# Optimization experiments

Hardware: AMD Instinct MI355X
Metric: run time of the kernel (lower is better)

The kernel has to match this reference:

```python
import jax, jax.numpy as jnp
import numpy as np

PH, PW, PS = 4, 4, 16          # patch grid h/w and patch_size
SEQ = PS * PS                  # 256 tokens per chunk
EH = EW = ET = 4               # mem_expand_size
RPW = 2 * EW + 1               # 9
RPH = 2 * EH + 1               # 9
RPF = RPH * RPW                # 81
HEADS, DHEAD, DIM = 16, 64, 1024
INNER = HEADS * DHEAD
SCALE = DHEAD ** -0.5


def _pos(idx):
    nf = PH * PW
    inner = idx % nf
    return inner % PH, inner // PH, idx // nf


def _rotary(freqs, t):
    # freqs: [n, rot_dim] broadcast over leading dims of t [..., n, rot_dim]
    x1 = t[..., 0::2]
    x2 = t[..., 1::2]
    rot = jnp.stack((-x2, x1), axis=-1).reshape(t.shape)
    return t * jnp.cos(freqs) + rot * jnp.sin(freqs)


def setup_inputs() -> dict:
    key = jax.random.key(0)
    ks = jax.random.split(key, 9)
    B, M, TXT = 16, 8, 77
    KV = M * SEQ + TXT
    return {
        "x": jax.random.normal(ks[0], (B, SEQ, DIM), jnp.float32),
        "cond": jax.random.normal(ks[1], (B, KV, DIM), jnp.float32),
        "freqs": jax.random.normal(ks[2], (PH * PS, PW * PS, DHEAD), jnp.float32),
        "Wq": jax.random.normal(ks[3], (DIM, INNER), jnp.float32) * 0.02,
        "Wk": jax.random.normal(ks[4], (DIM, INNER), jnp.float32) * 0.02,
        "Wv": jax.random.normal(ks[5], (DIM, INNER), jnp.float32) * 0.02,
        "rel_table": jax.random.normal(ks[6], (RPH * RPW * (2 * ET + 1), HEADS), jnp.float32) * 0.02,
        "Wo": jax.random.normal(ks[7], (INNER, DIM), jnp.float32) * 0.02,
        "bo": jax.random.normal(ks[8], (DIM,), jnp.float32) * 0.02,
        "mem_idxs": jnp.arange(8, dtype=jnp.int64) if jax.config.jax_enable_x64 else jnp.arange(8, dtype=jnp.int32),
        "cur_patch_idx": 21,
    }


def reference(x, cond, freqs, Wq, Wk, Wv, rel_table, Wo, bo, mem_idxs, cur_patch_idx):
    B = x.shape[0]
    M = mem_idxs.shape[0]
    MS = M * SEQ
    # QKV projections -> [b, h, n, d]
    q = (x @ Wq).reshape(B, SEQ, HEADS, DHEAD).transpose(0, 2, 1, 3)
    k = (cond @ Wk).reshape(B, -1, HEADS, DHEAD).transpose(0, 2, 1, 3)
    v = (cond @ Wv).reshape(B, -1, HEADS, DHEAD).transpose(0, 2, 1, 3)

    # relative position indices (gather into bias table)
    rs, cs, ts = _pos(cur_patch_idx)           # python ints (static)
    rt, ct, tt = _pos(mem_idxs)                # [M] arrays
    rel_idx = (rt - rs + EH) * RPW + (ct - cs + EW) + (tt - ts + ET) * RPF
    bias = rel_table[rel_idx]                  # [M, H]
    bias = jnp.repeat(bias.T, SEQ, axis=1)[None, :, :, None]  # [1, H, M*SEQ, 1]
    km = k[:, :, :MS] + bias                   # bias added to memory K before rotary

    # rotary freqs: source patch (static slice) and target patches (gathered)
    src = freqs[rs * PS:(rs + 1) * PS, cs * PS:(cs + 1) * PS].reshape(SEQ, -1)
    rows = rt[:, None] * PS + jnp.arange(PS)   # [M, PS]
    cols = ct[:, None] * PS + jnp.arange(PS)   # [M, PS]
    tgt = freqs[rows[:, :, None], cols[:, None, :]].reshape(MS, -1)  # [M*SEQ, rot]

    q = _rotary(src, q)
    km = _rotary(tgt, km)
    k = jnp.concatenate([km, k[:, :, MS:]], axis=2)

    dots = jnp.einsum('bhid,bhjd->bhij', q, k) * SCALE
    attn = jax.nn.softmax(dots, axis=-1)
    out = jnp.einsum('bhij,bhjd->bhid', attn, v)
    out = out.transpose(0, 2, 1, 3).reshape(B, SEQ, INNER)
    return out @ Wo + bo
```

## Files before the change

### kernel.cpp

```cpp
#include <hip/hip_runtime.h>
#include <cstdint>

typedef __bf16 bf16;
typedef bf16 bf16x2 __attribute__((ext_vector_type(2)));
typedef bf16 bf16x4 __attribute__((ext_vector_type(4)));
typedef bf16 bf16x8 __attribute__((ext_vector_type(8)));
typedef float floatx4 __attribute__((ext_vector_type(4)));

#define SEQ   256
#define DIMM  1024
#define HEADS 16
#define KV_LEN 2125
#define KV_PAD 2176
#define KV_BLKS 17
#define MS_TOK 2048
#define ATT_SCALE 0.125f
#define TILE_ELEMS (128 * 32)

__device__ __forceinline__ void load_lds16(const bf16* g, bf16* l) {
    __builtin_amdgcn_global_load_lds(
        (const __attribute__((address_space(1))) void*)g,
        (__attribute__((address_space(3))) void*)l, 16, 0, 0);
}

__global__ __launch_bounds__(256) void convert_kernel(
        const float* __restrict__ src, bf16* __restrict__ dst, long total) {
    long i4 = ((long)blockIdx.x * 256 + threadIdx.x) * 4;
    if (i4 >= total) return;
    const float4 v = *(const float4*)(src + i4);
    bf16x4 o;
    o[0] = (bf16)v.x; o[1] = (bf16)v.y; o[2] = (bf16)v.z; o[3] = (bf16)v.w;
    *(bf16x4*)(dst + i4) = o;
}

__global__ __launch_bounds__(256) void convert_cond_kernel(
        const float* __restrict__ src, bf16* __restrict__ dst, long total_dst) {
    long i4 = ((long)blockIdx.x * 256 + threadIdx.x) * 4;
    if (i4 >= total_dst) return;
    long drow = i4 >> 10;
    int b = (int)(drow / KV_PAD);
    int j = (int)(drow - (long)b * KV_PAD);
    bf16x4 o;
    if (j < KV_LEN) {
        long srow = (long)b * KV_LEN + j;
        const float4 v = *(const float4*)(src + (srow << 10) + (i4 & 1023));
        o[0] = (bf16)v.x; o[1] = (bf16)v.y; o[2] = (bf16)v.z; o[3] = (bf16)v.w;
    } else {
        o[0] = o[1] = o[2] = o[3] = (bf16)0.f;
    }
    *(bf16x4*)(dst + i4) = o;
}

__global__ __launch_bounds__(256) void transpose_bf16_kernel(
        const float* __restrict__ W, bf16* __restrict__ Wt, int N) {
    __shared__ float tile[32][33];
    int n0 = blockIdx.x * 32, k0 = blockIdx.y * 32;
    int r = threadIdx.x >> 5, c = threadIdx.x & 31;
    #pragma unroll
    for (int i = 0; i < 4; ++i)
        tile[r + i * 8][c] = W[(size_t)(k0 + r + i * 8) * N + n0 + c];
    __syncthreads();
    #pragma unroll
    for (int i = 0; i < 4; ++i)
        Wt[(size_t)(n0 + r + i * 8) * N + k0 + c] = (bf16)tile[c][r + i * 8];
}

__global__ __launch_bounds__(256) void rot_tables_kernel(
        const float* __restrict__ freqs, const float* __restrict__ rel_table,
        const int* __restrict__ mem_idxs, const int* __restrict__ cur,
        float* __restrict__ ckT, float* __restrict__ skT,
        float* __restrict__ cqT, float* __restrict__ sqT,
        float* __restrict__ biasK) {
    int t = blockIdx.x * 256 + threadIdx.x;
    const int cp = *cur; const int inner = cp & 15;
    const int rs = inner & 3, cs = inner >> 2, ts = cp >> 4;
    if (t < MS_TOK * 64) {
        int j = t >> 6, d = t & 63;
        int mi = mem_idxs[j >> 8];
        int rt = mi & 3, ct = (mi >> 2) & 3;
        int pidx = j & 255;
        int fr = rt * 16 + (pidx >> 4), fc = ct * 16 + (pidx & 15);
        float f = freqs[(size_t)(fr * 64 + fc) * 64 + d];
        ckT[t] = __cosf(f); skT[t] = __sinf(f);
    } else if (t < MS_TOK * 64 + SEQ * 64) {
        int t2 = t - MS_TOK * 64;
        int s = t2 >> 6, d = t2 & 63;
        int fr = rs * 16 + (s >> 4), fc = cs * 16 + (s & 15);
        float f = freqs[(size_t)(fr * 64 + fc) * 64 + d];
        cqT[t2] = __cosf(f); sqT[t2] = __sinf(f);
    } else if (t < MS_TOK * 64 + SEQ * 64 + 128) {
        int t3 = t - (MS_TOK * 64 + SEQ * 64);
        int m = t3 >> 4, h = t3 & 15;
        int mi = mem_idxs[m];
        int rt = mi & 3, ct = (mi >> 2) & 3, tt = mi >> 4;
        int rel = (rt - rs + 4) * 9 + (ct - cs + 4) + (tt - ts + 4) * 81;
        biasK[t3] = rel_table[rel * HEADS + h];
    }
}

__device__ __forceinline__ void gemm_loop_db(
        const bf16* __restrict__ Ag, const bf16* __restrict__ Bg, int K,
        bf16* __restrict__ As, bf16* __restrict__ Bs,
        floatx4 (&acc)[4][4]) {
    const int tid  = threadIdx.x;
    const int wave = tid >> 6, lane = tid & 63;
    const int quad = lane >> 4, l16 = lane & 15;
    const int wm = wave >> 1, wn = wave & 1;
    #pragma unroll
    for (int i = 0; i < 2; ++i) {
        int c = i * 256 + wave * 64 + lane;
        int r = c >> 2, c8 = (c & 3) * 8;
        load_lds16(Ag + (long)r * K + c8, As + (i * 256 + wave * 64) * 8);
        load_lds16(Bg + (long)r * K + c8, Bs + (i * 256 + wave * 64) * 8);
    }
    for (int k0 = 0; k0 < K; k0 += 32) {
        const int cur = (k0 >> 5) & 1;
        bf16* Asc = As + cur * TILE_ELEMS;
        bf16* Bsc = Bs + cur * TILE_ELEMS;
        __syncthreads();
        if (k0 + 32 < K) {
            bf16* Asn = As + (cur ^ 1) * TILE_ELEMS;
            bf16* Bsn = Bs + (cur ^ 1) * TILE_ELEMS;
            #pragma unroll
            for (int i = 0; i < 2; ++i) {
                int c = i * 256 + wave * 64 + lane;
                int r = c >> 2, c8 = (c & 3) * 8;
                load_lds16(Ag + (long)r * K + k0 + 32 + c8, Asn + (i * 256 + wave * 64) * 8);
                load_lds16(Bg + (long)r * K + k0 + 32 + c8, Bsn + (i * 256 + wave * 64) * 8);
            }
        }
        bf16x8 af[4], bfr[4];
        #pragma unroll
        for (int mt = 0; mt < 4; ++mt)
            af[mt] = *(const bf16x8*)(Asc + (wm * 64 + mt * 16 + l16) * 32 + quad * 8);
        #pragma unroll
        for (int nt = 0; nt < 4; ++nt)
            bfr[nt] = *(const bf16x8*)(Bsc + (wn * 64 + nt * 16 + l16) * 32 + quad * 8);
        #pragma unroll
        for (int mt = 0; mt < 4; ++mt)
            #pragma unroll
            for (int nt = 0; nt < 4; ++nt)
                acc[mt][nt] = __builtin_amdgcn_mfma_f32_16x16x32_bf16(af[mt], bfr[nt], acc[mt][nt], 0, 0, 0);
    }
}

__global__ __launch_bounds__(256) void gemm_o_kernel(
        const bf16* __restrict__ A, const bf16* __restrict__ Bt,
        float* __restrict__ Cout, const float* __restrict__ bias, int N) {
    __shared__ bf16 As[2 * TILE_ELEMS];
    __shared__ bf16 Bs[2 * TILE_ELEMS];
    const int tid  = threadIdx.x;
    const int wave = tid >> 6, lane = tid & 63;
    const int quad = lane >> 4, l16 = lane & 15;
    const int wm = wave >> 1, wn = wave & 1;
    const long row0 = (long)blockIdx.x * 128, col0 = (long)blockIdx.y * 128;
    floatx4 acc[4][4] = {};
    gemm_loop_db(A + row0 * DIMM, Bt + col0 * DIMM, DIMM, As, Bs, acc);
    #pragma unroll
    for (int mt = 0; mt < 4; ++mt) {
        #pragma unroll
        for (int nt = 0; nt < 4; ++nt) {
            long r = row0 + wm * 64 + mt * 16 + quad * 4;
            long ccol = col0 + wn * 64 + nt * 16 + l16;
            float bv = bias[ccol];
            #pragma unroll
            for (int i = 0; i < 4; ++i)
                Cout[(r + i) * (long)N + ccol] = acc[mt][nt][i] + bv;
        }
    }
}

__global__ __launch_bounds__(256) void gemm_q_rot_kernel(
        const bf16* __restrict__ A, const bf16* __restrict__ Bt,
        bf16* __restrict__ Qout, const float* __restrict__ cqT,
        const float* __restrict__ sqT) {
    __shared__ bf16 As[2 * TILE_ELEMS];
    __shared__ bf16 Bs[2 * TILE_ELEMS];
    const int tid  = threadIdx.x;
    const int wave = tid >> 6, lane = tid & 63;
    const int quad = lane >> 4, l16 = lane & 15;
    const int wm = wave >> 1, wn = wave & 1;
    const long row0 = (long)blockIdx.x * 128, col0 = (long)blockIdx.y * 128;
    floatx4 acc[4][4] = {};
    gemm_loop_db(A + row0 * DIMM, Bt + col0 * DIMM, DIMM, As, Bs, acc);
    #pragma unroll
    for (int mt = 0; mt < 4; ++mt) {
        #pragma unroll
        for (int nt = 0; nt < 4; ++nt) {
            long rr = row0 + wm * 64 + mt * 16 + quad * 4;
            int ccol = (int)col0 + wn * 64 + nt * 16 + l16;
            int d = ccol & 63;
            #pragma unroll
            for (int i = 0; i < 4; ++i) {
                long r = rr + i; int s = (int)(r & 255);
                float c_ = cqT[s * 64 + d], s_ = sqT[s * 64 + d];
                float q = acc[mt][nt][i];
                float pn = __shfl_xor(q, 1);
                float outv = (d & 1) ? (q * c_ + pn * s_) : (q * c_ - pn * s_);
                Qout[r * DIMM + ccol] = (bf16)outv;
            }
        }
    }
}

__global__ __launch_bounds__(256) void gemm_k_kernel(
        const bf16* __restrict__ A, const bf16* __restrict__ Btk,
        bf16* __restrict__ Kout, const float* __restrict__ ckT,
        const float* __restrict__ skT, const float* __restrict__ biasK) {
    __shared__ bf16 As[2 * TILE_ELEMS];
    __shared__ bf16 Bs[2 * TILE_ELEMS];
    const int tid  = threadIdx.x;
    const int wave = tid >> 6, lane = tid & 63;
    const int quad = lane >> 4, l16 = lane & 15;
    const int wm = wave >> 1, wn = wave & 1;
    const long row0 = (long)blockIdx.x * 128, col0 = (long)blockIdx.y * 128;
    floatx4 acc[4][4] = {};
    gemm_loop_db(A + row0 * DIMM, Btk + col0 * DIMM, DIMM, As, Bs, acc);
    const int bidx = (int)(row0 / KV_PAD);
    #pragma unroll
    for (int mt = 0; mt < 4; ++mt) {
        #pragma unroll
        for (int nt = 0; nt < 4; ++nt) {
            long rr = row0 + wm * 64 + mt * 16 + quad * 4;
            int ccol = (int)col0 + wn * 64 + nt * 16 + l16;
            int h = ccol >> 6, d = ccol & 63;
            int jbase = (int)(rr - (long)bidx * KV_PAD);
            #pragma unroll
            for (int i = 0; i < 4; ++i) {
                int j = jbase + i;
                float kb = acc[mt][nt][i];
                float c_ = 1.f, s_ = 0.f;
                if (j < MS_TOK) {
                    kb += biasK[((j >> 8) << 4) + h];
                    c_ = ckT[j * 64 + d]; s_ = skT[j * 64 + d];
                }
                float pn = __shfl_xor(kb, 1);
                float outv = (d & 1) ? (kb * c_ + pn * s_) : (kb * c_ - pn * s_);
                Kout[(rr + i) * DIMM + ccol] = (bf16)outv;
            }
        }
    }
}

__global__ __launch_bounds__(256) void gemm_vt_kernel(
        const bf16* __restrict__ Wvt, const bf16* __restrict__ condb,
        bf16* __restrict__ VT) {
    __shared__ bf16 As[2 * TILE_ELEMS];
    __shared__ bf16 Bs[2 * TILE_ELEMS];
    const int tid  = threadIdx.x;
    const int wave = tid >> 6, lane = tid & 63;
    const int quad = lane >> 4, l16 = lane & 15;
    const int wm = wave >> 1, wn = wave & 1;
    const int b  = blockIdx.y / KV_BLKS, tb = blockIdx.y % KV_BLKS;
    const long row0 = (long)blockIdx.x * 128;
    const long col0 = (long)tb * 128;
    const bf16* Bt = condb + (size_t)b * KV_PAD * DIMM;
    floatx4 acc[4][4] = {};
    gemm_loop_db(Wvt + row0 * DIMM, Bt + col0 * DIMM, DIMM, As, Bs, acc);
    #pragma unroll
    for (int mt = 0; mt < 4; ++mt) {
        #pragma unroll
        for (int nt = 0; nt < 4; ++nt) {
            long f0 = row0 + wm * 64 + mt * 16 + quad * 4;
            long t0 = col0 + wn * 64 + nt * 16 + l16;
            #pragma unroll
            for (int i = 0; i < 4; ++i)
                VT[((size_t)b * DIMM + f0 + i) * KV_PAD + t0] = (bf16)acc[mt][nt][i];
        }
    }
}

__global__ __launch_bounds__(256, 3) void attn_kernel(
        const bf16* __restrict__ Qb, const bf16* __restrict__ Kb,
        const bf16* __restrict__ VT, bf16* __restrict__ Ob) {
    const int bh = blockIdx.x & 255, qt = blockIdx.x >> 8;
    const int b = bh >> 4, h = bh & 15;
    const int tid = threadIdx.x, wave = tid >> 6, lane = tid & 63;
    const int quad = lane >> 4, l16 = lane & 15;
    __shared__ bf16 Ks[128 * 72];
    __shared__ bf16 Vt[64 * 144];
    __shared__ bf16 Ps[4][16 * 72];

    const int qrow0 = b * SEQ + qt * 64 + wave * 16;
    const bf16* qp = Qb + (size_t)(qrow0 + l16) * DIMM + h * 64 + quad * 8;
    bf16x8 qf0 = *(const bf16x8*)(qp);
    bf16x8 qf1 = *(const bf16x8*)(qp + 32);

    floatx4 oacc[4] = {};
    floatx4 lacc = {};
    bf16x8 ones;
    #pragma unroll
    for (int t = 0; t < 8; ++t) ones[t] = (bf16)1.0f;

    const size_t kbase = ((size_t)b * KV_PAD) * DIMM + h * 64;
    const size_t vbase = ((size_t)(bh * 64)) * KV_PAD;

    const int kchunk = tid & 1;
    const int gl = tid >> 1;
    const int g  = ((gl & 31) << 2) | (gl >> 5);
    const int gg = g & 63;
    const int dstrow = (g >> 6) * 64 + ((gg & 3) << 4) + (gg >> 2);
    const int vd = tid >> 2, vseg = tid & 3;

    bf16x8 kr[4], vr[4];
    {
        int jr = g; if (jr > KV_LEN - 1) jr = KV_LEN - 1;
        const bf16* gp = Kb + kbase + (size_t)jr * DIMM + kchunk * 32;
        kr[0] = *(const bf16x8*)(gp);      kr[1] = *(const bf16x8*)(gp + 8);
        kr[2] = *(const bf16x8*)(gp + 16); kr[3] = *(const bf16x8*)(gp + 24);
        const bf16* vp = VT + vbase + (size_t)vd * KV_PAD + vseg * 32;
        vr[0] = *(const bf16x8*)(vp);      vr[1] = *(const bf16x8*)(vp + 8);
        vr[2] = *(const bf16x8*)(vp + 16); vr[3] = *(const bf16x8*)(vp + 24);
    }

    for (int j0 = 0; j0 < KV_LEN; j0 += 128) {
        __syncthreads();
        {
            bf16* dp = Ks + dstrow * 72 + kchunk * 32;
            *(bf16x8*)(dp)      = kr[0]; *(bf16x8*)(dp + 8)  = kr[1];
            *(bf16x8*)(dp + 16) = kr[2]; *(bf16x8*)(dp + 24) = kr[3];
            bf16* dv = Vt + vd * 144 + vseg * 32;
            *(bf16x8*)(dv)      = vr[0]; *(bf16x8*)(dv + 8)  = vr[1];
            *(bf16x8*)(dv + 16) = vr[2]; *(bf16x8*)(dv + 24) = vr[3];
        }
        __syncthreads();
        if (j0 + 128 < KV_LEN) {
            int jr = j0 + 128 + g; if (jr > KV_LEN - 1) jr = KV_LEN - 1;
            const bf16* gp = Kb + kbase + (size_t)jr * DIMM + kchunk * 32;
            kr[0] = *(const bf16x8*)(gp);      kr[1] = *(const bf16x8*)(gp + 8);
            kr[2] = *(const bf16x8*)(gp + 16); kr[3] = *(const bf16x8*)(gp + 24);
            const bf16* vp = VT + vbase + (size_t)vd * KV_PAD + j0 + 128 + vseg * 32;
            vr[0] = *(const bf16x8*)(vp);      vr[1] = *(const bf16x8*)(vp + 8);
            vr[2] = *(const bf16x8*)(vp + 16); vr[3] = *(const bf16x8*)(vp + 24);
        }
        #pragma unroll
        for (int c = 0; c < 2; ++c) {
            floatx4 s[4] = {};
            #pragma unroll
            for (int jt = 0; jt < 4; ++jt) {
                const bf16* kp = Ks + (c * 64 + jt * 16 + l16) * 72 + quad * 8;
                bf16x8 kb0 = *(const bf16x8*)(kp);
                bf16x8 kb1 = *(const bf16x8*)(kp + 32);
                s[jt] = __builtin_amdgcn_mfma_f32_16x16x32_bf16(qf0, kb0, s[jt], 0, 0, 0);
                s[jt] = __builtin_amdgcn_mfma_f32_16x16x32_bf16(qf1, kb1, s[jt], 0, 0, 0);
            }
            const int colbase = j0 + c * 64 + 4 * l16;
            #pragma unroll
            for (int r = 0; r < 4; ++r) {
                bf16x4 pk;
                #pragma unroll
                for (int jt = 0; jt < 4; ++jt) {
                    bool ok = (colbase + jt) < KV_LEN;
                    float p = ok ? __expf(s[jt][r] * ATT_SCALE) : 0.f;
                    pk[jt] = (bf16)p;
                }
                *(bf16x4*)(&Ps[wave][(quad * 4 + r) * 72 + l16 * 4]) = pk;
            }
            #pragma unroll
            for (int kf = 0; kf < 2; ++kf) {
                bf16x8 pa = *(const bf16x8*)(&Ps[wave][l16 * 72 + kf * 32 + quad * 8]);
                lacc = __builtin_amdgcn_mfma_f32_16x16x32_bf16(pa, ones, lacc, 0, 0, 0);
                #pragma unroll
                for (int dt = 0; dt < 4; ++dt) {
                    bf16x8 vb = *(const bf16x8*)(Vt + (dt * 16 + l16) * 144 + c * 64 + kf * 32 + quad * 8);
                    oacc[dt] = __builtin_amdgcn_mfma_f32_16x16x32_bf16(pa, vb, oacc[dt], 0, 0, 0);
                }
            }
        }
    }
    #pragma unroll
    for (int r = 0; r < 4; ++r) {
        float inv = 1.f / lacc[r];
        size_t orow = (size_t)(qrow0 + quad * 4 + r) * DIMM + h * 64;
        #pragma unroll
        for (int dt = 0; dt < 4; ++dt)
            Ob[orow + dt * 16 + l16] = (bf16)(oacc[dt][r] * inv);
    }
}

extern "C" void kernel_launch(void* const* d_in, const int* in_sizes, int n_in,
                              void* d_out, int out_size, void* d_ws, size_t ws_size,
                              hipStream_t stream) {
    const float* x     = (const float*)d_in[0];
    const float* cond  = (const float*)d_in[1];
    const float* freqs = (const float*)d_in[2];
    const float* Wq    = (const float*)d_in[3];
    const float* Wk    = (const float*)d_in[4];
    const float* Wv    = (const float*)d_in[5];
    const float* rel   = (const float*)d_in[6];
    const float* Wo    = (const float*)d_in[7];
    const float* bo    = (const float*)d_in[8];
    const int* mem_idxs = (const int*)d_in[9];
    const int* cur      = (const int*)d_in[10];
    float* out = (float*)d_out;

    const int B   = 16;
    const int Mq  = B * SEQ;
    const int Mkv_pad = B * KV_PAD;

    char* ws = (char*)d_ws;
    size_t off = 0;
    auto alloc = [&](size_t bytes) { void* pp = ws + off; off = (off + bytes + 255) & ~(size_t)255; return pp; };
    bf16* xb    = (bf16*)alloc((size_t)Mq * DIMM * 2);
    bf16* condb = (bf16*)alloc((size_t)Mkv_pad * DIMM * 2);
    bf16* Wqt   = (bf16*)alloc((size_t)DIMM * DIMM * 2);
    bf16* Wkt   = (bf16*)alloc((size_t)DIMM * DIMM * 2);
    bf16* Wvt   = (bf16*)alloc((size_t)DIMM * DIMM * 2);
    bf16* Wot   = (bf16*)alloc((size_t)DIMM * DIMM * 2);
    bf16* Qb    = (bf16*)alloc((size_t)Mq * DIMM * 2);
    bf16* Kb    = (bf16*)alloc((size_t)Mkv_pad * DIMM * 2);
    bf16* VTb   = (bf16*)alloc((size_t)B * DIMM * KV_PAD * 2);
    bf16* Ab    = (bf16*)alloc((size_t)Mq * DIMM * 2);
    float* ckT  = (float*)alloc((size_t)MS_TOK * 64 * 4);
    float* skT  = (float*)alloc((size_t)MS_TOK * 64 * 4);
    float* cqT  = (float*)alloc((size_t)SEQ * 64 * 4);
    float* sqT  = (float*)alloc((size_t)SEQ * 64 * 4);
    float* biasK = (float*)alloc(128 * 4);

    long xtot = (long)Mq * DIMM;
    convert_kernel<<<(int)((xtot / 4 + 255) / 256), 256, 0, stream>>>(x, xb, xtot);
    long ctot = (long)Mkv_pad * DIMM;
    convert_cond_kernel<<<(int)((ctot / 4 + 255) / 256), 256, 0, stream>>>(cond, condb, ctot);
    dim3 tg(32, 32);
    transpose_bf16_kernel<<<tg, 256, 0, stream>>>(Wq, Wqt, DIMM);
    transpose_bf16_kernel<<<tg, 256, 0, stream>>>(Wk, Wkt, DIMM);
    transpose_bf16_kernel<<<tg, 256, 0, stream>>>(Wv, Wvt, DIMM);
    transpose_bf16_kernel<<<tg, 256, 0, stream>>>(Wo, Wot, DIMM);

    int ttot = MS_TOK * 64 + SEQ * 64 + 128;
    rot_tables_kernel<<<(ttot + 255) / 256, 256, 0, stream>>>(
        freqs, rel, mem_idxs, cur, ckT, skT, cqT, sqT, biasK);

    gemm_q_rot_kernel<<<dim3(Mq / 128, 8), 256, 0, stream>>>(xb, Wqt, Qb, cqT, sqT);
    gemm_k_kernel<<<dim3(Mkv_pad / 128, 8), 256, 0, stream>>>(condb, Wkt, Kb, ckT, skT, biasK);
    gemm_vt_kernel<<<dim3(8, B * KV_BLKS), 256, 0, stream>>>(Wvt, condb, VTb);

    attn_kernel<<<4 * B * HEADS, 256, 0, stream>>>(Qb, Kb, VTb, Ab);

    gemm_o_kernel<<<dim3(Mq / 128, 8), 256, 0, stream>>>(Ab, Wot, out, bo, DIMM);
}
```

Before: 624.5 us.

## Use 256x256 tiles with 512-thread blocks for K and V projection GEMMs

Result: slower. 734.9 us (+17.7%).

```diff
diff --git a/kernel.cpp b/kernel.cpp
--- a/kernel.cpp
+++ b/kernel.cpp
@@ -13,9 +13,11 @@
 #define KV_LEN 2125
 #define KV_PAD 2176
 #define KV_BLKS 17
+#define VT_NBLK 9
 #define MS_TOK 2048
 #define ATT_SCALE 0.125f
 #define TILE_ELEMS (128 * 32)
+#define TILE2_ELEMS (256 * 32)
 
 __device__ __forceinline__ void load_lds16(const bf16* g, bf16* l) {
     __builtin_amdgcn_global_load_lds(
@@ -144,6 +146,52 @@
     }
 }
 
+__device__ __forceinline__ void gemm_loop_256(
+        const bf16* __restrict__ Ag, const bf16* __restrict__ Bg, int K,
+        bf16* __restrict__ As, bf16* __restrict__ Bs,
+        floatx4 (&acc)[8][4]) {
+    const int tid  = threadIdx.x;
+    const int wave = tid >> 6, lane = tid & 63;
+    const int quad = lane >> 4, l16 = lane & 15;
+    const int wm = wave >> 2, wn = wave & 3;
+    #pragma unroll
+    for (int i = 0; i < 2; ++i) {
+        int c = i * 512 + tid;
+        int r = c >> 2, c8 = (c & 3) * 8;
+        load_lds16(Ag + (long)r * K + c8, As + (i * 512 + wave * 64) * 8);
+        load_lds16(Bg + (long)r * K + c8, Bs + (i * 512 + wave * 64) * 8);
+    }
+    for (int k0 = 0; k0 < K; k0 += 32) {
+        const int cur = (k0 >> 5) & 1;
+        bf16* Asc = As + cur * TILE2_ELEMS;
+        bf16* Bsc = Bs + cur * TILE2_ELEMS;
+        __syncthreads();
+        if (k0 + 32 < K) {
+            bf16* Asn = As + (cur ^ 1) * TILE2_ELEMS;
+            bf16* Bsn = Bs + (cur ^ 1) * TILE2_ELEMS;
+            #pragma unroll
+            for (int i = 0; i < 2; ++i) {
+                int c = i * 512 + tid;
+                int r = c >> 2, c8 = (c & 3) * 8;
+                load_lds16(Ag + (long)r * K + k0 + 32 + c8, Asn + (i * 512 + wave * 64) * 8);
+                load_lds16(Bg + (long)r * K + k0 + 32 + c8, Bsn + (i * 512 + wave * 64) * 8);
+            }
+        }
+        bf16x8 af[8], bfr[4];
+        #pragma unroll
+        for (int mt = 0; mt < 8; ++mt)
+            af[mt] = *(const bf16x8*)(Asc + (wm * 128 + mt * 16 + l16) * 32 + quad * 8);
+        #pragma unroll
+        for (int nt = 0; nt < 4; ++nt)
+            bfr[nt] = *(const bf16x8*)(Bsc + (wn * 64 + nt * 16 + l16) * 32 + quad * 8);
+        #pragma unroll
+        for (int mt = 0; mt < 8; ++mt)
+            #pragma unroll
+            for (int nt = 0; nt < 4; ++nt)
+                acc[mt][nt] = __builtin_amdgcn_mfma_f32_16x16x32_bf16(af[mt], bfr[nt], acc[mt][nt], 0, 0, 0);
+    }
+}
+
 __global__ __launch_bounds__(256) void gemm_o_kernel(
         const bf16* __restrict__ A, const bf16* __restrict__ Bt,
         float* __restrict__ Cout, const float* __restrict__ bias, int N) {
@@ -203,28 +251,28 @@
     }
 }
 
-__global__ __launch_bounds__(256) void gemm_k_kernel(
+__global__ __launch_bounds__(512, 2) void gemm_k_kernel(
         const bf16* __restrict__ A, const bf16* __restrict__ Btk,
         bf16* __restrict__ Kout, const float* __restrict__ ckT,
         const float* __restrict__ skT, const float* __restrict__ biasK) {
-    __shared__ bf16 As[2 * TILE_ELEMS];
-    __shared__ bf16 Bs[2 * TILE_ELEMS];
-    const int tid  = threadIdx.x;
-    const int wave = tid >> 6, lane = tid & 63;
-    const int quad = lane >> 4, l16 = lane & 15;
-    const int wm = wave >> 1, wn = wave & 1;
-    const long row0 = (long)blockIdx.x * 128, col0 = (long)blockIdx.y * 128;
-    floatx4 acc[4][4] = {};
-    gemm_loop_db(A + row0 * DIMM, Btk + col0 * DIMM, DIMM, As, Bs, acc);
-    const int bidx = (int)(row0 / KV_PAD);
-    #pragma unroll
-    for (int mt = 0; mt < 4; ++mt) {
+    __shared__ bf16 As[2 * TILE2_ELEMS];
+    __shared__ bf16 Bs[2 * TILE2_ELEMS];
+    const int tid  = threadIdx.x;
+    const int wave = tid >> 6, lane = tid & 63;
+    const int quad = lane >> 4, l16 = lane & 15;
+    const int wm = wave >> 2, wn = wave & 3;
+    const long row0 = (long)blockIdx.x * 256, col0 = (long)blockIdx.y * 256;
+    floatx4 acc[8][4] = {};
+    gemm_loop_256(A + row0 * DIMM, Btk + col0 * DIMM, DIMM, As, Bs, acc);
+    #pragma unroll
+    for (int mt = 0; mt < 8; ++mt) {
         #pragma unroll
         for (int nt = 0; nt < 4; ++nt) {
-            long rr = row0 + wm * 64 + mt * 16 + quad * 4;
+            int rr = (int)row0 + wm * 128 + mt * 16 + quad * 4;
             int ccol = (int)col0 + wn * 64 + nt * 16 + l16;
             int h = ccol >> 6, d = ccol & 63;
-            int jbase = (int)(rr - (long)bidx * KV_PAD);
+            int bidx = rr / KV_PAD;
+            int jbase = rr - bidx * KV_PAD;
             #pragma unroll
             for (int i = 0; i < 4; ++i) {
                 int j = jbase + i;
@@ -236,36 +284,39 @@
                 }
                 float pn = __shfl_xor(kb, 1);
                 float outv = (d & 1) ? (kb * c_ + pn * s_) : (kb * c_ - pn * s_);
-                Kout[(rr + i) * DIMM + ccol] = (bf16)outv;
-            }
-        }
-    }
-}
-
-__global__ __launch_bounds__(256) void gemm_vt_kernel(
+                Kout[(long)(rr + i) * DIMM + ccol] = (bf16)outv;
+            }
+        }
+    }
+}
+
+__global__ __launch_bounds__(512, 2) void gemm_vt_kernel(
         const bf16* __restrict__ Wvt, const bf16* __restrict__ condb,
         bf16* __restrict__ VT) {
-    __shared__ bf16 As[2 * TILE_ELEMS];
-    __shared__ bf16 Bs[2 * TILE_ELEMS];
-    const int tid  = threadIdx.x;
-    const int wave = tid >> 6, lane = tid & 63;
-    const int quad = lane >> 4, l16 = lane & 15;
-    const int wm = wave >> 1, wn = wave & 1;
-    const int b  = blockIdx.y / KV_BLKS, tb = blockIdx.y % KV_BLKS;
-    const long row0 = (long)blockIdx.x * 128;
-    const long col0 = (long)tb * 128;
+    __shared__ bf16 As[2 * TILE2_ELEMS];
+    __shared__ bf16 Bs[2 * TILE2_ELEMS];
+    const int tid  = threadIdx.x;
+    const int wave = tid >> 6, lane = tid & 63;
+    const int quad = lane >> 4, l16 = lane & 15;
+    const int wm = wave >> 2, wn = wave & 3;
+    const int b  = blockIdx.y / VT_NBLK, tb = blockIdx.y % VT_NBLK;
+    const long row0 = (long)blockIdx.x * 256;
+    const long col0 = (long)tb * 256;
     const bf16* Bt = condb + (size_t)b * KV_PAD * DIMM;
-    floatx4 acc[4][4] = {};
-    gemm_loop_db(Wvt + row0 * DIMM, Bt + col0 * DIMM, DIMM, As, Bs, acc);
-    #pragma unroll
-    for (int mt = 0; mt < 4; ++mt) {
+    floatx4 acc[8][4] = {};
+    gemm_loop_256(Wvt + row0 * DIMM, Bt + col0 * DIMM, DIMM, As, Bs, acc);
+    #pragma unroll
+    for (int mt = 0; mt < 8; ++mt) {
         #pragma unroll
         for (int nt = 0; nt < 4; ++nt) {
-            long f0 = row0 + wm * 64 + mt * 16 + quad * 4;
-            long t0 = col0 + wn * 64 + nt * 16 + l16;
-            #pragma unroll
-            for (int i = 0; i < 4; ++i)
-                VT[((size_t)b * DIMM + f0 + i) * KV_PAD + t0] = (bf16)acc[mt][nt][i];
+            int tfrag = (int)col0 + wn * 64 + nt * 16;
+            if (tfrag < KV_PAD) {
+                long f0 = row0 + wm * 128 + mt * 16 + quad * 4;
+                long t0 = tfrag + l16;
+                #pragma unroll
+                for (int i = 0; i < 4; ++i)
+                    VT[((size_t)b * DIMM + f0 + i) * KV_PAD + t0] = (bf16)acc[mt][nt][i];
+            }
         }
     }
 }
@@ -432,8 +483,8 @@
         freqs, rel, mem_idxs, cur, ckT, skT, cqT, sqT, biasK);
 
     gemm_q_rot_kernel<<<dim3(Mq / 128, 8), 256, 0, stream>>>(xb, Wqt, Qb, cqT, sqT);
-    gemm_k_kernel<<<dim3(Mkv_pad / 128, 8), 256, 0, stream>>>(condb, Wkt, Kb, ckT, skT, biasK);
-    gemm_vt_kernel<<<dim3(8, B * KV_BLKS), 256, 0, stream>>>(Wvt, condb, VTb);
+    gemm_k_kernel<<<dim3(Mkv_pad / 256, DIMM / 256), 512, 0, stream>>>(condb, Wkt, Kb, ckT, skT, biasK);
+    gemm_vt_kernel<<<dim3(DIMM / 256, B * VT_NBLK), 512, 0, stream>>>(Wvt, condb, VTb);
 
     attn_kernel<<<4 * B * HEADS, 256, 0, stream>>>(Qb, Kb, VTb, Ab);
 
```
